# Kernel tuning notes

Hardware: AMD Instinct MI355X
Metric: run time of the kernel (lower is better)

Reference implementation:

```python
import jax, jax.numpy as jnp
import numpy as np

N_NODES = 100000


def sage_conv(x, src, dst, counts, Wl, bl, Wr):
    # mean-aggregate source features into destination nodes
    msg_sum = jax.ops.segment_sum(x[src], dst, num_segments=N_NODES)  # [N, d]
    aggr = msg_sum / counts  # zero-degree nodes stay 0 (counts clamped to 1)
    return aggr @ Wl + bl + x @ Wr


def setup_inputs() -> dict:
    key = jax.random.key(0)
    ks = jax.random.split(key, 16)
    N, E, IN, H, OUT = N_NODES, 640000, 128, 128, 40
    x = jax.random.normal(ks[0], (N, IN), dtype=jnp.float32)
    edge_index = jax.random.randint(ks[1], (2, E), 0, N, dtype=jnp.int64)

    def lin(k, fan_in, fan_out):
        s = 1.0 / np.sqrt(fan_in)
        return jax.random.uniform(k, (fan_in, fan_out), jnp.float32, -s, s)

    return {
        "x": x,
        "edge_index": edge_index,
        "W1l": lin(ks[2], IN, H), "b1": jnp.zeros((H,), jnp.float32), "W1r": lin(ks[3], IN, H),
        "W2l": lin(ks[4], H, H), "b2": jnp.zeros((H,), jnp.float32), "W2r": lin(ks[5], H, H),
        "W3l": lin(ks[6], H, H), "b3": jnp.zeros((H,), jnp.float32), "W3r": lin(ks[7], H, H),
        "Wf1": lin(ks[8], H, H), "bf1": jnp.zeros((H,), jnp.float32),
        "Wf2": lin(ks[9], H, OUT), "bf2": jnp.zeros((OUT,), jnp.float32),
    }


def reference(x, edge_index, W1l, b1, W1r, W2l, b2, W2r, W3l, b3, W3r, Wf1, bf1, Wf2, bf2):
    src, dst = edge_index[0], edge_index[1]
    counts = jax.ops.segment_sum(jnp.ones_like(dst, dtype=x.dtype), dst,
                                 num_segments=N_NODES)
    counts = jnp.maximum(counts, 1.0)[:, None]  # [N, 1]

    h = jax.nn.relu(sage_conv(x, src, dst, counts, W1l, b1, W1r))
    h = jax.nn.relu(sage_conv(h, src, dst, counts, W2l, b2, W2r))
    h = sage_conv(h, src, dst, counts, W3l, b3, W3r)

    z = jax.nn.relu(h @ Wf1 + bf1) @ Wf2 + bf2  # [N, out]
    return jax.nn.log_softmax(z, axis=1), h
```

## Files before the change

kernel.cpp:

```cpp
#include <hip/hip_runtime.h>
#include <math.h>

#define N_NODES 100000
#define HDIM    128
#define ODIM    40
#define NBLK    ((N_NODES + 255) / 256)

typedef unsigned short u16;
typedef unsigned int   u32;
typedef short bf16x8 __attribute__((ext_vector_type(8)));
typedef float f32x4  __attribute__((ext_vector_type(4)));

__device__ inline float bf16lo_to_f(u32 v) {
    u32 u = v << 16; float f; __builtin_memcpy(&f, &u, 4); return f;
}
__device__ inline float bf16hi_to_f(u32 v) {
    u32 u = v & 0xffff0000u; float f; __builtin_memcpy(&f, &u, 4); return f;
}
__device__ inline u16 f_to_bf16(float f) {
    u32 u; __builtin_memcpy(&u, &f, 4);
    u32 r = (u + 0x7fffu + ((u >> 16) & 1u)) >> 16;
    return (u16)r;
}
__device__ inline u32 pack_bf16x2(float a, float b) {
    return (u32)f_to_bf16(a) | ((u32)f_to_bf16(b) << 16);
}

__global__ __launch_bounds__(256) void count_deg_kernel(
    const int* __restrict__ dst, int* __restrict__ ic, int E)
{
    int e = blockIdx.x * 256 + threadIdx.x;
    if (e < E) atomicAdd(ic + dst[e], 1);
}

__global__ __launch_bounds__(256) void block_sum_kernel(
    const int* __restrict__ ic, int* __restrict__ bs, int n)
{
    __shared__ int sm[256];
    int t = threadIdx.x;
    int i = blockIdx.x * 256 + t;
    sm[t] = (i < n) ? ic[i] : 0;
    __syncthreads();
    for (int s = 128; s > 0; s >>= 1) {
        if (t < s) sm[t] += sm[t + s];
        __syncthreads();
    }
    if (t == 0) bs[blockIdx.x] = sm[0];
}

__global__ __launch_bounds__(512) void scan_bs_kernel(int* __restrict__ bs, int nb)
{
    __shared__ int sm[512];
    int t = threadIdx.x;
    sm[t] = (t < nb) ? bs[t] : 0;
    __syncthreads();
    for (int off = 1; off < 512; off <<= 1) {
        int v = (t >= off) ? sm[t - off] : 0;
        __syncthreads();
        sm[t] += v;
        __syncthreads();
    }
    if (t < nb) bs[t] = (t == 0) ? 0 : sm[t - 1];
}

__global__ __launch_bounds__(256) void scan_block_kernel(
    const int* __restrict__ ic, const int* __restrict__ bs,
    int* __restrict__ pc, int n)
{
    __shared__ int sm[256];
    int t = threadIdx.x;
    int i = blockIdx.x * 256 + t;
    int v = (i < n) ? ic[i] : 0;
    sm[t] = v;
    __syncthreads();
    for (int off = 1; off < 256; off <<= 1) {
        int u = (t >= off) ? sm[t - off] : 0;
        __syncthreads();
        sm[t] += u;
        __syncthreads();
    }
    if (i < n) pc[i] = bs[blockIdx.x] + sm[t] - v;
}

__global__ __launch_bounds__(256) void fill_kernel(
    const int* __restrict__ src, const int* __restrict__ dst,
    int* __restrict__ pc, int* __restrict__ cs, int E)
{
    int e = blockIdx.x * 256 + threadIdx.x;
    if (e < E) {
        int p = atomicAdd(pc + dst[e], 1);
        cs[p] = src[e];
    }
}

__global__ __launch_bounds__(256) void f2bf_kernel(
    const float2* __restrict__ in, u32* __restrict__ out, int n2)
{
    int i = blockIdx.x * 256 + threadIdx.x;
    if (i < n2) { float2 v = in[i]; out[i] = pack_bf16x2(v.x, v.y); }
}

struct WPtrs { const float* w[7]; };

__global__ __launch_bounds__(256) void pack_w_kernel(WPtrs p, u16* __restrict__ out)
{
    int mat = blockIdx.y;
    int e = blockIdx.x * 256 + threadIdx.x;
    int k = e >> 7, n = e & 127;
    float v = p.w[mat][e];
    int nt = n >> 4, ks = k >> 5, q = (k >> 3) & 3, j = k & 7;
    int dst = mat * 16384 + (((nt * 4 + ks) * 64 + q * 16 + (n & 15)) << 3) + j;
    out[dst] = f_to_bf16(v);
}

__global__ __launch_bounds__(256) void pack_wf2_kernel(
    const float* __restrict__ Wf2, u16* __restrict__ outp)
{
    int e = blockIdx.x * 256 + threadIdx.x;
    if (e >= 128 * 48) return;
    int k = e / 48, n = e - k * 48;
    float v = (n < ODIM) ? Wf2[k * ODIM + n] : 0.f;
    int nt = n >> 4, ks = k >> 5, q = (k >> 3) & 3, j = k & 7;
    outp[(((nt * 4 + ks) * 64 + q * 16 + (n & 15)) << 3) + j] = f_to_bf16(v);
}

__global__ __launch_bounds__(256) void gather_mean_grp_kernel(
    const u32* __restrict__ feat,
    const int* __restrict__ cs, const int* __restrict__ pc, const int* __restrict__ ic,
    u32* __restrict__ A)
{
    const int grp  = threadIdx.x >> 4;
    const int ch   = threadIdx.x & 15;
    const int node = blockIdx.x * 16 + grp;
    const int end  = pc[node];
    const int deg  = ic[node];
    const int start = end - deg;

    const u32* fb = feat + (ch << 2);

    float acc[8] = {0.f,0.f,0.f,0.f,0.f,0.f,0.f,0.f};
    const uint4 Z = {0u, 0u, 0u, 0u};

    if (deg > 0) {
        uint4 c0 = *reinterpret_cast<const uint4*>(fb + ((size_t)cs[start] << 6));
        uint4 c1 = (deg > 1)
            ? *reinterpret_cast<const uint4*>(fb + ((size_t)cs[start + 1] << 6)) : Z;
        for (int j = 0; j < deg; ++j) {
            uint4 n = (j + 2 < deg)
                ? *reinterpret_cast<const uint4*>(fb + ((size_t)cs[start + j + 2] << 6)) : Z;
            acc[0] += bf16lo_to_f(c0.x); acc[1] += bf16hi_to_f(c0.x);
            acc[2] += bf16lo_to_f(c0.y); acc[3] += bf16hi_to_f(c0.y);
            acc[4] += bf16lo_to_f(c0.z); acc[5] += bf16hi_to_f(c0.z);
            acc[6] += bf16lo_to_f(c0.w); acc[7] += bf16hi_to_f(c0.w);
            c0 = c1; c1 = n;
        }
    }

    float inv = 1.0f / (float)(deg > 0 ? deg : 1);
    uint4 o;
    o.x = pack_bf16x2(acc[0] * inv, acc[1] * inv);
    o.y = pack_bf16x2(acc[2] * inv, acc[3] * inv);
    o.z = pack_bf16x2(acc[4] * inv, acc[5] * inv);
    o.w = pack_bf16x2(acc[6] * inv, acc[7] * inv);
    *reinterpret_cast<uint4*>(A + ((size_t)node << 6) + (ch << 2)) = o;
}

__device__ inline void stage_tile_async(
    const u16* __restrict__ Ain, u16* __restrict__ sDst,
    int base, int wave, int lane)
{
    #pragma unroll
    for (int it = 0; it < 4; ++it) {
        int s   = (wave * 4 + it) * 64 + lane;
        int row = ((s >> 8) << 4) | (s & 15);
        int ch8 = (((s >> 6) & 3) << 2) | ((s >> 4) & 3);
        int rowg = base + row; if (rowg > N_NODES - 1) rowg = N_NODES - 1;
        __builtin_amdgcn_global_load_lds(
            (const __attribute__((address_space(1))) void*)(Ain + ((size_t)rowg << 7) + (ch8 << 3)),
            (__attribute__((address_space(3))) void*)(sDst + ((wave * 4 + it) << 9)),
            16, 0, 0);
    }
}

__global__ __launch_bounds__(256) void mfma_gemm_kernel(
    const u16* __restrict__ A1, const u16* __restrict__ A2,
    const u16* __restrict__ W1p, const u16* __restrict__ W2p,
    const float* __restrict__ bias,
    u16* __restrict__ out16, float* __restrict__ out32, int do_relu)
{
    __shared__ __align__(16) u16 sAll[2 * 8192];
    const int tid  = threadIdx.x;
    const int base = blockIdx.x * 64;
    const int nmats = (A2 != nullptr) ? 2 : 1;
    const int wave = tid >> 6;
    const int lane = tid & 63;

    stage_tile_async(A1, &sAll[0], base, wave, lane);
    if (nmats == 2) stage_tile_async(A2, &sAll[8192], base, wave, lane);
    __syncthreads();

    f32x4 acc[8];
    #pragma unroll
    for (int nt = 0; nt < 8; ++nt) acc[nt] = (f32x4){0.f, 0.f, 0.f, 0.f};

    for (int mat = 0; mat < nmats; ++mat) {
        const u16* Wp = mat ? W2p : W1p;
        const u16* sA = &sAll[mat * 8192];
        #pragma unroll
        for (int ks = 0; ks < 4; ++ks) {
            bf16x8 a = *reinterpret_cast<const bf16x8*>(sA + (((wave * 4 + ks) * 64 + lane) << 3));
            #pragma unroll
            for (int nt = 0; nt < 8; ++nt) {
                bf16x8 b = *reinterpret_cast<const bf16x8*>(Wp + (((nt * 4 + ks) * 64 + lane) << 3));
                acc[nt] = __builtin_amdgcn_mfma_f32_16x16x32_bf16(a, b, acc[nt], 0, 0, 0);
            }
        }
    }
    __syncthreads();

    u16* sOut = sAll;
    const int m = lane & 15;
    const int q = lane >> 4;
    #pragma unroll
    for (int nt = 0; nt < 8; ++nt) {
        int col = nt * 16 + m;
        float bv = bias[col];
        #pragma unroll
        for (int r = 0; r < 4; ++r) {
            float v = acc[nt][r] + bv;
            if (do_relu) v = fmaxf(v, 0.f);
            int row = wave * 16 + q * 4 + r;
            sOut[row * 136 + col] = f_to_bf16(v);
            if (out32) {
                int rowg = base + row;
                if (rowg < N_NODES) out32[((size_t)rowg << 7) + col] = v;
            }
        }
    }
    __syncthreads();

    if (out16) {
        #pragma unroll
        for (int it = 0; it < 4; ++it) {
            int c = it * 256 + tid;
            int row = c >> 4, ch = c & 15;
            int rowg = base + row;
            if (rowg < N_NODES)
                *reinterpret_cast<uint4*>(out16 + ((size_t)rowg << 7) + (ch << 3)) =
                    *reinterpret_cast<const uint4*>(sOut + row * 136 + (ch << 3));
        }
    }
}

__global__ __launch_bounds__(256) void mfma_head_kernel(
    const u16* __restrict__ h3,
    const u16* __restrict__ Wf1p, const float* __restrict__ bf1,
    const u16* __restrict__ Wf2p, const float* __restrict__ bf2,
    float* __restrict__ out)
{
    __shared__ __align__(16) u16 sA[8192];
    const int tid  = threadIdx.x;
    const int base = blockIdx.x * 64;
    const int wave = tid >> 6;
    const int lane = tid & 63;

    stage_tile_async(h3, sA, base, wave, lane);
    __syncthreads();

    f32x4 acc[8];
    #pragma unroll
    for (int nt = 0; nt < 8; ++nt) acc[nt] = (f32x4){0.f, 0.f, 0.f, 0.f};
    #pragma unroll
    for (int ks = 0; ks < 4; ++ks) {
        bf16x8 a = *reinterpret_cast<const bf16x8*>(sA + (((wave * 4 + ks) * 64 + lane) << 3));
        #pragma unroll
        for (int nt = 0; nt < 8; ++nt) {
            bf16x8 b = *reinterpret_cast<const bf16x8*>(Wf1p + (((nt * 4 + ks) * 64 + lane) << 3));
            acc[nt] = __builtin_amdgcn_mfma_f32_16x16x32_bf16(a, b, acc[nt], 0, 0, 0);
        }
    }
    __syncthreads();

    const int m = lane & 15;
    const int q = lane >> 4;
    #pragma unroll
    for (int nt = 0; nt < 8; ++nt) {
        int col = nt * 16 + m;
        float bv = bf1[col];
        #pragma unroll
        for (int r = 0; r < 4; ++r) {
            float v = fmaxf(acc[nt][r] + bv, 0.f);
            int dc = (wave * 4 + (nt >> 1)) * 64 + ((nt & 1) * 2 + (m >> 3)) * 16 + (q * 4 + r);
            sA[(dc << 3) | (m & 7)] = f_to_bf16(v);
        }
    }
    __syncthreads();

    f32x4 acc2[3];
    #pragma unroll
    for (int nt = 0; nt < 3; ++nt) acc2[nt] = (f32x4){0.f, 0.f, 0.f, 0.f};
    #pragma unroll
    for (int ks = 0; ks < 4; ++ks) {
        bf16x8 a = *reinterpret_cast<const bf16x8*>(sA + (((wave * 4 + ks) * 64 + lane) << 3));
        #pragma unroll
        for (int nt = 0; nt < 3; ++nt) {
            bf16x8 b = *reinterpret_cast<const bf16x8*>(Wf2p + (((nt * 4 + ks) * 64 + lane) << 3));
            acc2[nt] = __builtin_amdgcn_mfma_f32_16x16x32_bf16(a, b, acc2[nt], 0, 0, 0);
        }
    }

    float z[3][4];
    float mx[4] = {-INFINITY, -INFINITY, -INFINITY, -INFINITY};
    #pragma unroll
    for (int nt = 0; nt < 3; ++nt) {
        int col = nt * 16 + m;
        bool valid = (col < ODIM);
        float bv = valid ? bf2[col] : 0.f;
        #pragma unroll
        for (int r = 0; r < 4; ++r) {
            z[nt][r] = acc2[nt][r] + bv;
            if (valid) mx[r] = fmaxf(mx[r], z[nt][r]);
        }
    }
    #pragma unroll
    for (int off = 1; off < 16; off <<= 1) {
        #pragma unroll
        for (int r = 0; r < 4; ++r) mx[r] = fmaxf(mx[r], __shfl_xor(mx[r], off, 16));
    }
    float sum[4] = {0.f, 0.f, 0.f, 0.f};
    #pragma unroll
    for (int nt = 0; nt < 3; ++nt) {
        int col = nt * 16 + m;
        if (col < ODIM) {
            #pragma unroll
            for (int r = 0; r < 4; ++r) sum[r] += expf(z[nt][r] - mx[r]);
        }
    }
    #pragma unroll
    for (int off = 1; off < 16; off <<= 1) {
        #pragma unroll
        for (int r = 0; r < 4; ++r) sum[r] += __shfl_xor(sum[r], off, 16);
    }
    float lse[4];
    #pragma unroll
    for (int r = 0; r < 4; ++r) lse[r] = logf(sum[r]) + mx[r];

    #pragma unroll
    for (int nt = 0; nt < 3; ++nt) {
        int col = nt * 16 + m;
        if (col >= ODIM) continue;
        #pragma unroll
        for (int r = 0; r < 4; ++r) {
            int rowg = base + wave * 16 + q * 4 + r;
            if (rowg >= N_NODES) continue;
            out[(size_t)rowg * ODIM + col] = z[nt][r] - lse[r];
        }
    }
}

extern "C" void kernel_launch(void* const* d_in, const int* in_sizes, int n_in,
                              void* d_out, int out_size, void* d_ws, size_t ws_size,
                              hipStream_t stream) {
    const float* x   = (const float*)d_in[0];
    const int*   ei  = (const int*)d_in[1];
    const int E = in_sizes[1] / 2;
    const int* src = ei;
    const int* dst = ei + E;

    const float* W1l = (const float*)d_in[2];
    const float* b1  = (const float*)d_in[3];
    const float* W1r = (const float*)d_in[4];
    const float* W2l = (const float*)d_in[5];
    const float* b2  = (const float*)d_in[6];
    const float* W2r = (const float*)d_in[7];
    const float* W3l = (const float*)d_in[8];
    const float* b3  = (const float*)d_in[9];
    const float* W3r = (const float*)d_in[10];
    const float* Wf1 = (const float*)d_in[11];
    const float* bf1 = (const float*)d_in[12];
    const float* Wf2 = (const float*)d_in[13];
    const float* bf2 = (const float*)d_in[14];

    float* out     = (float*)d_out;
    float* outTail = out + (size_t)N_NODES * ODIM;

    int* ic = (int*)out;
    int* pc = ic + 100352;
    int* bs = pc + 100352;
    int* cs = bs + 1024;

    const size_t FEAT16 = (size_t)N_NODES * HDIM;
    u16* X16  = (u16*)d_ws;
    u16* F16a = X16  + FEAT16;
    u16* F16b = F16a + FEAT16;
    u16* A16  = F16b + FEAT16;
    u16* Wpk  = A16  + FEAT16;
    u16* Wp_1l = Wpk + 0 * 16384;
    u16* Wp_1r = Wpk + 1 * 16384;
    u16* Wp_2l = Wpk + 2 * 16384;
    u16* Wp_2r = Wpk + 3 * 16384;
    u16* Wp_3l = Wpk + 4 * 16384;
    u16* Wp_3r = Wpk + 5 * 16384;
    u16* Wp_f1 = Wpk + 6 * 16384;
    u16* Wf2p  = Wpk + 7 * 16384;

    const int gemmGrid   = (N_NODES + 63) / 64;
    const int gatherGrid = N_NODES / 16;
    const int edgeGrid   = (E + 255) / 256;
    const int cvtGrid    = (N_NODES * HDIM / 2 + 255) / 256;

    hipMemsetAsync(ic, 0, N_NODES * sizeof(int), stream);
    count_deg_kernel<<<edgeGrid, 256, 0, stream>>>(dst, ic, E);
    block_sum_kernel<<<NBLK, 256, 0, stream>>>(ic, bs, N_NODES);
    scan_bs_kernel<<<1, 512, 0, stream>>>(bs, NBLK);
    scan_block_kernel<<<NBLK, 256, 0, stream>>>(ic, bs, pc, N_NODES);
    fill_kernel<<<edgeGrid, 256, 0, stream>>>(src, dst, pc, cs, E);

    f2bf_kernel<<<cvtGrid, 256, 0, stream>>>((const float2*)x, (u32*)X16, N_NODES * HDIM / 2);
    WPtrs wp; wp.w[0] = W1l; wp.w[1] = W1r; wp.w[2] = W2l; wp.w[3] = W2r;
    wp.w[4] = W3l; wp.w[5] = W3r; wp.w[6] = Wf1;
    pack_w_kernel<<<dim3(64, 7), 256, 0, stream>>>(wp, Wpk);
    pack_wf2_kernel<<<24, 256, 0, stream>>>(Wf2, Wf2p);

    gather_mean_grp_kernel<<<gatherGrid, 256, 0, stream>>>((const u32*)X16, cs, pc, ic, (u32*)A16);
    mfma_gemm_kernel<<<gemmGrid, 256, 0, stream>>>(A16, X16, Wp_1l, Wp_1r, b1, F16a, nullptr, 1);

    gather_mean_grp_kernel<<<gatherGrid, 256, 0, stream>>>((const u32*)F16a, cs, pc, ic, (u32*)A16);
    mfma_gemm_kernel<<<gemmGrid, 256, 0, stream>>>(A16, F16a, Wp_2l, Wp_2r, b2, F16b, nullptr, 1);

    gather_mean_grp_kernel<<<gatherGrid, 256, 0, stream>>>((const u32*)F16b, cs, pc, ic, (u32*)A16);
    mfma_gemm_kernel<<<gemmGrid, 256, 0, stream>>>(A16, F16b, Wp_3l, Wp_3r, b3, F16a, outTail, 0);

    mfma_head_kernel<<<gemmGrid, 256, 0, stream>>>(F16a, Wp_f1, bf1, Wf2p, bf2, out);
}
```

Baseline: 421.1 us.

## Stage weights in LDS and load activations directly into registers in GEMMs

The SAGE GEMM kernel now loads A-operand fragments straight from global memory into registers and stages the packed weight matrix in LDS, so every block reuses it. Each block now covers 128 rows (two 16-row tiles per wave) instead of 64, doubling weight reuse per LDS load. The head kernel likewise stages Wf1 and Wf2 in LDS rather than reading weights from global memory inside the MFMA loop. This trades higher register and LDS use for fewer global weight reads, and may reduce occupancy.

```diff
diff --git a/kernel.cpp b/kernel.cpp
--- a/kernel.cpp
+++ b/kernel.cpp
@@ -165,75 +165,100 @@
     *reinterpret_cast<uint4*>(A + ((size_t)node << 6) + (ch << 2)) = o;
 }
 
-__device__ inline void stage_tile_async(
-    const u16* __restrict__ Ain, u16* __restrict__ sDst,
-    int base, int wave, int lane)
-{
-    #pragma unroll
-    for (int it = 0; it < 4; ++it) {
-        int s   = (wave * 4 + it) * 64 + lane;
-        int row = ((s >> 8) << 4) | (s & 15);
-        int ch8 = (((s >> 6) & 3) << 2) | ((s >> 4) & 3);
-        int rowg = base + row; if (rowg > N_NODES - 1) rowg = N_NODES - 1;
-        __builtin_amdgcn_global_load_lds(
-            (const __attribute__((address_space(1))) void*)(Ain + ((size_t)rowg << 7) + (ch8 << 3)),
-            (__attribute__((address_space(3))) void*)(sDst + ((wave * 4 + it) << 9)),
-            16, 0, 0);
-    }
-}
-
 __global__ __launch_bounds__(256) void mfma_gemm_kernel(
     const u16* __restrict__ A1, const u16* __restrict__ A2,
     const u16* __restrict__ W1p, const u16* __restrict__ W2p,
     const float* __restrict__ bias,
     u16* __restrict__ out16, float* __restrict__ out32, int do_relu)
 {
-    __shared__ __align__(16) u16 sAll[2 * 8192];
+    __shared__ __align__(16) u16 sBuf[128 * 136];
     const int tid  = threadIdx.x;
-    const int base = blockIdx.x * 64;
-    const int nmats = (A2 != nullptr) ? 2 : 1;
     const int wave = tid >> 6;
     const int lane = tid & 63;
-
-    stage_tile_async(A1, &sAll[0], base, wave, lane);
-    if (nmats == 2) stage_tile_async(A2, &sAll[8192], base, wave, lane);
-    __syncthreads();
-
-    f32x4 acc[8];
-    #pragma unroll
-    for (int nt = 0; nt < 8; ++nt) acc[nt] = (f32x4){0.f, 0.f, 0.f, 0.f};
-
-    for (int mat = 0; mat < nmats; ++mat) {
-        const u16* Wp = mat ? W2p : W1p;
-        const u16* sA = &sAll[mat * 8192];
+    const int m = lane & 15;
+    const int q = lane >> 4;
+    const int base = blockIdx.x * 128;
+
+    int row0 = base + wave * 16 + m;        if (row0 > N_NODES - 1) row0 = N_NODES - 1;
+    int row1 = base + (wave + 4) * 16 + m;  if (row1 > N_NODES - 1) row1 = N_NODES - 1;
+
+    f32x4 acc0[8], acc1[8];
+    #pragma unroll
+    for (int nt = 0; nt < 8; ++nt) {
+        acc0[nt] = (f32x4){0.f, 0.f, 0.f, 0.f};
+        acc1[nt] = (f32x4){0.f, 0.f, 0.f, 0.f};
+    }
+
+    bf16x8 a0[4], a1[4];
+    #pragma unroll
+    for (int ks = 0; ks < 4; ++ks) {
+        a0[ks] = *reinterpret_cast<const bf16x8*>(A1 + ((size_t)row0 << 7) + ((ks * 4 + q) << 3));
+        a1[ks] = *reinterpret_cast<const bf16x8*>(A1 + ((size_t)row1 << 7) + ((ks * 4 + q) << 3));
+    }
+    #pragma unroll
+    for (int it = 0; it < 8; ++it) {
+        int off = (it * 4 + wave) << 9;
+        __builtin_amdgcn_global_load_lds(
+            (const __attribute__((address_space(1))) void*)(W1p + off + (lane << 3)),
+            (__attribute__((address_space(3))) void*)(sBuf + off), 16, 0, 0);
+    }
+    __syncthreads();
+
+    #pragma unroll
+    for (int ks = 0; ks < 4; ++ks) {
+        #pragma unroll
+        for (int nt = 0; nt < 8; ++nt) {
+            bf16x8 b = *reinterpret_cast<const bf16x8*>(sBuf + (((nt * 4 + ks) * 64 + lane) << 3));
+            acc0[nt] = __builtin_amdgcn_mfma_f32_16x16x32_bf16(a0[ks], b, acc0[nt], 0, 0, 0);
+            acc1[nt] = __builtin_amdgcn_mfma_f32_16x16x32_bf16(a1[ks], b, acc1[nt], 0, 0, 0);
+        }
+    }
+
+    if (A2 != nullptr) {
+        __syncthreads();
         #pragma unroll
         for (int ks = 0; ks < 4; ++ks) {
-            bf16x8 a = *reinterpret_cast<const bf16x8*>(sA + (((wave * 4 + ks) * 64 + lane) << 3));
+            a0[ks] = *reinterpret_cast<const bf16x8*>(A2 + ((size_t)row0 << 7) + ((ks * 4 + q) << 3));
+            a1[ks] = *reinterpret_cast<const bf16x8*>(A2 + ((size_t)row1 << 7) + ((ks * 4 + q) << 3));
+        }
+        #pragma unroll
+        for (int it = 0; it < 8; ++it) {
+            int off = (it * 4 + wave) << 9;
+            __builtin_amdgcn_global_load_lds(
+                (const __attribute__((address_space(1))) void*)(W2p + off + (lane << 3)),
+                (__attribute__((address_space(3))) void*)(sBuf + off), 16, 0, 0);
+        }
+        __syncthreads();
+
+        #pragma unroll
+        for (int ks = 0; ks < 4; ++ks) {
             #pragma unroll
             for (int nt = 0; nt < 8; ++nt) {
-                bf16x8 b = *reinterpret_cast<const bf16x8*>(Wp + (((nt * 4 + ks) * 64 + lane) << 3));
-                acc[nt] = __builtin_amdgcn_mfma_f32_16x16x32_bf16(a, b, acc[nt], 0, 0, 0);
+                bf16x8 b = *reinterpret_cast<const bf16x8*>(sBuf + (((nt * 4 + ks) * 64 + lane) << 3));
+                acc0[nt] = __builtin_amdgcn_mfma_f32_16x16x32_bf16(a0[ks], b, acc0[nt], 0, 0, 0);
+                acc1[nt] = __builtin_amdgcn_mfma_f32_16x16x32_bf16(a1[ks], b, acc1[nt], 0, 0, 0);
             }
         }
     }
     __syncthreads();
 
-    u16* sOut = sAll;
-    const int m = lane & 15;
-    const int q = lane >> 4;
     #pragma unroll
     for (int nt = 0; nt < 8; ++nt) {
         int col = nt * 16 + m;
         float bv = bias[col];
         #pragma unroll
         for (int r = 0; r < 4; ++r) {
-            float v = acc[nt][r] + bv;
-            if (do_relu) v = fmaxf(v, 0.f);
-            int row = wave * 16 + q * 4 + r;
-            sOut[row * 136 + col] = f_to_bf16(v);
+            float v0 = acc0[nt][r] + bv;
+            float v1 = acc1[nt][r] + bv;
+            if (do_relu) { v0 = fmaxf(v0, 0.f); v1 = fmaxf(v1, 0.f); }
+            int rl0 = wave * 16 + q * 4 + r;
+            int rl1 = rl0 + 64;
+            sBuf[rl0 * 136 + col] = f_to_bf16(v0);
+            sBuf[rl1 * 136 + col] = f_to_bf16(v1);
             if (out32) {
-                int rowg = base + row;
-                if (rowg < N_NODES) out32[((size_t)rowg << 7) + col] = v;
+                int rg0 = base + rl0, rg1 = base + rl1;
+                if (rg0 < N_NODES) out32[((size_t)rg0 << 7) + col] = v0;
+                if (rg1 < N_NODES) out32[((size_t)rg1 << 7) + col] = v1;
             }
         }
     }
@@ -241,13 +266,13 @@
 
     if (out16) {
         #pragma unroll
-        for (int it = 0; it < 4; ++it) {
+        for (int it = 0; it < 8; ++it) {
             int c = it * 256 + tid;
             int row = c >> 4, ch = c & 15;
             int rowg = base + row;
             if (rowg < N_NODES)
                 *reinterpret_cast<uint4*>(out16 + ((size_t)rowg << 7) + (ch << 3)) =
-                    *reinterpret_cast<const uint4*>(sOut + row * 136 + (ch << 3));
+                    *reinterpret_cast<const uint4*>(sBuf + row * 136 + (ch << 3));
         }
     }
 }
@@ -258,31 +283,51 @@
     const u16* __restrict__ Wf2p, const float* __restrict__ bf2,
     float* __restrict__ out)
 {
-    __shared__ __align__(16) u16 sA[8192];
+    __shared__ __align__(16) u16 sW1[16384];
+    __shared__ __align__(16) u16 sW2[6144];
     const int tid  = threadIdx.x;
     const int base = blockIdx.x * 64;
     const int wave = tid >> 6;
     const int lane = tid & 63;
-
-    stage_tile_async(h3, sA, base, wave, lane);
-    __syncthreads();
-
-    f32x4 acc[8];
-    #pragma unroll
-    for (int nt = 0; nt < 8; ++nt) acc[nt] = (f32x4){0.f, 0.f, 0.f, 0.f};
-    #pragma unroll
-    for (int ks = 0; ks < 4; ++ks) {
-        bf16x8 a = *reinterpret_cast<const bf16x8*>(sA + (((wave * 4 + ks) * 64 + lane) << 3));
-        #pragma unroll
-        for (int nt = 0; nt < 8; ++nt) {
-            bf16x8 b = *reinterpret_cast<const bf16x8*>(Wf1p + (((nt * 4 + ks) * 64 + lane) << 3));
-            acc[nt] = __builtin_amdgcn_mfma_f32_16x16x32_bf16(a, b, acc[nt], 0, 0, 0);
-        }
-    }
-    __syncthreads();
-
     const int m = lane & 15;
     const int q = lane >> 4;
+
+    int row = base + wave * 16 + m; if (row > N_NODES - 1) row = N_NODES - 1;
+
+    bf16x8 a[4];
+    #pragma unroll
+    for (int ks = 0; ks < 4; ++ks)
+        a[ks] = *reinterpret_cast<const bf16x8*>(h3 + ((size_t)row << 7) + ((ks * 4 + q) << 3));
+
+    #pragma unroll
+    for (int it = 0; it < 8; ++it) {
+        int off = (it * 4 + wave) << 9;
+        __builtin_amdgcn_global_load_lds(
+            (const __attribute__((address_space(1))) void*)(Wf1p + off + (lane << 3)),
+            (__attribute__((address_space(3))) void*)(sW1 + off), 16, 0, 0);
+    }
+    #pragma unroll
+    for (int it = 0; it < 3; ++it) {
+        int off = (it * 4 + wave) << 9;
+        __builtin_amdgcn_global_load_lds(
+            (const __attribute__((address_space(1))) void*)(Wf2p + off + (lane << 3)),
+            (__attribute__((address_space(3))) void*)(sW2 + off), 16, 0, 0);
+    }
+    __syncthreads();
+
+    f32x4 acc[8];
+    #pragma unroll
+    for (int nt = 0; nt < 8; ++nt) acc[nt] = (f32x4){0.f, 0.f, 0.f, 0.f};
+    #pragma unroll
+    for (int ks = 0; ks < 4; ++ks) {
+        #pragma unroll
+        for (int nt = 0; nt < 8; ++nt) {
+            bf16x8 b = *reinterpret_cast<const bf16x8*>(sW1 + (((nt * 4 + ks) * 64 + lane) << 3));
+            acc[nt] = __builtin_amdgcn_mfma_f32_16x16x32_bf16(a[ks], b, acc[nt], 0, 0, 0);
+        }
+    }
+    __syncthreads();
+
     #pragma unroll
     for (int nt = 0; nt < 8; ++nt) {
         int col = nt * 16 + m;
@@ -291,7 +336,7 @@
         for (int r = 0; r < 4; ++r) {
             float v = fmaxf(acc[nt][r] + bv, 0.f);
             int dc = (wave * 4 + (nt >> 1)) * 64 + ((nt & 1) * 2 + (m >> 3)) * 16 + (q * 4 + r);
-            sA[(dc << 3) | (m & 7)] = f_to_bf16(v);
+            sW1[(dc << 3) | (m & 7)] = f_to_bf16(v);
         }
     }
     __syncthreads();
@@ -301,11 +346,11 @@
     for (int nt = 0; nt < 3; ++nt) acc2[nt] = (f32x4){0.f, 0.f, 0.f, 0.f};
     #pragma unroll
     for (int ks = 0; ks < 4; ++ks) {
-        bf16x8 a = *reinterpret_cast<const bf16x8*>(sA + (((wave * 4 + ks) * 64 + lane) << 3));
+        bf16x8 a2 = *reinterpret_cast<const bf16x8*>(sW1 + (((wave * 4 + ks) * 64 + lane) << 3));
         #pragma unroll
         for (int nt = 0; nt < 3; ++nt) {
-            bf16x8 b = *reinterpret_cast<const bf16x8*>(Wf2p + (((nt * 4 + ks) * 64 + lane) << 3));
-            acc2[nt] = __builtin_amdgcn_mfma_f32_16x16x32_bf16(a, b, acc2[nt], 0, 0, 0);
+            bf16x8 b = *reinterpret_cast<const bf16x8*>(sW2 + (((nt * 4 + ks) * 64 + lane) << 3));
+            acc2[nt] = __builtin_amdgcn_mfma_f32_16x16x32_bf16(a2, b, acc2[nt], 0, 0, 0);
         }
     }
 
@@ -404,7 +449,8 @@
     u16* Wp_f1 = Wpk + 6 * 16384;
     u16* Wf2p  = Wpk + 7 * 16384;
 
-    const int gemmGrid   = (N_NODES + 63) / 64;
+    const int gemmGrid   = (N_NODES + 127) / 128;
+    const int headGrid   = (N_NODES + 63) / 64;
     const int gatherGrid = N_NODES / 16;
     const int edgeGrid   = (E + 255) / 256;
     const int cvtGrid    = (N_NODES * HDIM / 2 + 255) / 256;
@@ -431,5 +477,5 @@
     gather_mean_grp_kernel<<<gatherGrid, 256, 0, stream>>>((const u32*)F16b, cs, pc, ic, (u32*)A16);
     mfma_gemm_kernel<<<gemmGrid, 256, 0, stream>>>(A16, F16b, Wp_3l, Wp_3r, b3, F16a, outTail, 0);
 
-    mfma_head_kernel<<<gemmGrid, 256, 0, stream>>>(F16a, Wp_f1, bf1, Wf2p, bf2, out);
-}
+    mfma_head_kernel<<<headGrid, 256, 0, stream>>>(F16a, Wp_f1, bf1, Wf2p, bf2, out);
+}
```

Measured after the change: 402.1 us. 4.5% less time.
